# Kernel tuning notes

Measured on AMD Instinct MI355X. Metric: run time of the kernel, lower is better.

## Reference

```python
import jax, jax.numpy as jnp
import numpy as np

N, E, EP, D = 50000, 600000, 200000, 128
L = 3  # gnn layers


def _w(k, shape):
    # Kaiming-ish init: scale by 1/sqrt(fan_in)
    return jax.random.normal(k, shape, jnp.float32) / jnp.sqrt(jnp.float32(shape[-2]))


def setup_inputs() -> dict:
    key = jax.random.key(0)
    ks = jax.random.split(key, 20)
    x = jax.random.normal(ks[0], (N, D), jnp.float32)
    edge_attr = jax.random.normal(ks[1], (E, 1), jnp.float32)
    edge_index = jax.random.randint(ks[2], (2, E), 0, N, jnp.int64)
    predict_edge_index = jax.random.randint(ks[3], (2, EP), 0, N, jnp.int64)
    return {
        "x": x,
        "edge_attr": edge_attr,
        "edge_index": edge_index,
        "predict_edge_index": predict_edge_index,
        # SAGEConv params per layer: out = lin_l(mean_aggr) + lin_r(x); lin_r has no bias
        "Wl": _w(ks[4], (L, D, D)),
        "bl": jnp.zeros((L, D), jnp.float32),
        "Wr": _w(ks[5], (L, D, D)),
        # edge update MLPs: layer0 in=2D+1, layers 1..L-1 in=3D
        "euW0": _w(ks[6], (2 * D + 1, D)),
        "euB0": jnp.zeros((D,), jnp.float32),
        "euW": _w(ks[7], (L - 1, 3 * D, D)),
        "euB": jnp.zeros((L - 1, D), jnp.float32),
        # node post MLP
        "pW1": _w(ks[8], (D, D)), "pb1": jnp.zeros((D,), jnp.float32),
        "pW2": _w(ks[9], (D, D)), "pb2": jnp.zeros((D,), jnp.float32),
        # edge predict MLP (predict_mode=0: concat of two node embeddings)
        "qW1": _w(ks[10], (2 * D, D)), "qb1": jnp.zeros((D,), jnp.float32),
        "qW2": _w(ks[11], (D, 1)), "qb2": jnp.zeros((1,), jnp.float32),
    }


def reference(x, edge_attr, edge_index, predict_edge_index,
              Wl, bl, Wr, euW0, euB0, euW, euB,
              pW1, pb1, pW2, pb2, qW1, qb1, qW2, qb2):
    # dropout p=0.0 / eval mode -> identity
    src, dst = edge_index[0], edge_index[1]
    n = x.shape[0]
    deg = jax.ops.segment_sum(jnp.ones(src.shape, jnp.float32), dst, num_segments=n)
    deg = jnp.maximum(deg, 1.0)[:, None]
    for l in range(L):
        # SAGEConv: mean-aggregate source features at destinations
        aggr = jax.ops.segment_sum(x[src], dst, num_segments=n) / deg
        x = jax.nn.relu(aggr @ Wl[l] + bl[l] + x @ Wr[l])
        # edge update: gather endpoints, concat with edge_attr, Linear+ReLU (+outer relu no-op)
        cat = jnp.concatenate([x[src], x[dst], edge_attr], axis=-1)
        if l == 0:
            edge_attr = jax.nn.relu(cat @ euW0 + euB0)
        else:
            edge_attr = jax.nn.relu(cat @ euW[l - 1] + euB[l - 1])
    # node post MLP
    x = jax.nn.relu(x @ pW1 + pb1) @ pW2 + pb2
    # predict_mode=0: gather pair endpoints and score
    xi = x[predict_edge_index[0]]
    xj = x[predict_edge_index[1]]
    h = jnp.concatenate([xi, xj], axis=-1)
    y = jax.nn.relu(h @ qW1 + qb1) @ qW2 + qb2  # [EP, 1]
    return y
```

## Files before the change

kernel.cpp:

```cpp
#include <hip/hip_runtime.h>


typedef __attribute__((ext_vector_type(8))) short bf16x8;
typedef __attribute__((ext_vector_type(4))) float f32x4;

__device__ __forceinline__ unsigned short f2bf(float x) {
  unsigned u = __float_as_uint(x);
  u += 0x7fffu + ((u >> 16) & 1u);
  return (unsigned short)(u >> 16);
}
__device__ __forceinline__ float bf2f(unsigned short h) {
  return __uint_as_float(((unsigned)h) << 16);
}
__device__ __forceinline__ float lo16f(unsigned u) { return __uint_as_float(u << 16); }
__device__ __forceinline__ float hi16f(unsigned u) { return __uint_as_float(u & 0xffff0000u); }

__device__ __forceinline__ void gload_lds16(const void* g, void* l) {
  __builtin_amdgcn_global_load_lds(
      (const __attribute__((address_space(1))) unsigned int*)g,
      (__attribute__((address_space(3))) unsigned int*)l, 16, 0, 0);
}

__global__ void k_count(const int* __restrict__ dst, int* __restrict__ cnt, int E) {
  int i = blockIdx.x * blockDim.x + threadIdx.x;
  if (i < E) atomicAdd(&cnt[dst[i]], 1);
}

__global__ void k_scan1(const int* __restrict__ cnt, int* __restrict__ rs,
                        float* __restrict__ degf, int* __restrict__ bsum, int n) {
  __shared__ int wsum[16];
  __shared__ int wpre[16];
  const int tid = threadIdx.x;
  const int lane = tid & 63;
  const int wv = tid >> 6;
  int i = blockIdx.x * 1024 + tid;
  int v = (i < n) ? cnt[i] : 0;
  int s = v;
#pragma unroll
  for (int off = 1; off < 64; off <<= 1) {
    int t = __shfl_up(s, off);
    if (lane >= off) s += t;
  }
  if (lane == 63) wsum[wv] = s;
  __syncthreads();
  if (tid < 16) {
    int t = wsum[tid];
    int ss = t;
#pragma unroll
    for (int off = 1; off < 16; off <<= 1) {
      int u = __shfl_up(ss, off);
      if (tid >= off) ss += u;
    }
    wpre[tid] = ss - t;
  }
  __syncthreads();
  if (i < n) {
    rs[i] = s - v + wpre[wv];
    degf[i] = (float)(v > 0 ? v : 1);
  }
  if (tid == 1023) bsum[blockIdx.x] = wpre[15] + wsum[15];
}

__global__ void k_scan3(int* __restrict__ rs, const int* __restrict__ bsum,
                        int* __restrict__ cursor, int n, int nb) {
  __shared__ int boff_s[64];
  __shared__ int total_s;
  int tid = threadIdx.x;
  if (tid < 64) {
    int v = (tid < nb) ? bsum[tid] : 0;
    int s = v;
#pragma unroll
    for (int off = 1; off < 64; off <<= 1) {
      int t = __shfl_up(s, off);
      if (tid >= off) s += t;
    }
    boff_s[tid] = s - v;
    if (tid == 63) total_s = s;
  }
  __syncthreads();
  int i = blockIdx.x * blockDim.x + tid;
  if (i < n) {
    int r = rs[i] + boff_s[i >> 10];
    rs[i] = r;
    cursor[i] = r;
  }
  if (blockIdx.x == 0 && tid == 0) rs[n] = total_s;
}

__global__ void k_scatter(const int* __restrict__ src, const int* __restrict__ dst,
                          int* __restrict__ cursor, int* __restrict__ csr, int E) {
  int i = blockIdx.x * blockDim.x + threadIdx.x;
  if (i < E) {
    int p = atomicAdd(&cursor[dst[i]], 1);
    csr[p] = src[i];
  }
}

__global__ void k_split(const float* __restrict__ x, unsigned* __restrict__ X,
                        long n2) {
  long g = (long)blockIdx.x * blockDim.x + threadIdx.x;
  if (g >= n2) return;
  float2 v = ((const float2*)x)[g];
  unsigned short hx = f2bf(v.x), hy = f2bf(v.y);
  unsigned short lx = f2bf(v.x - bf2f(hx)), ly = f2bf(v.y - bf2f(hy));
  long row = g >> 6, p = g & 63;
  X[row * 128 + p] = (unsigned)hx | ((unsigned)hy << 16);
  X[row * 128 + 64 + p] = (unsigned)lx | ((unsigned)ly << 16);
}

__global__ void k_packAll(const float* __restrict__ Wl, const float* __restrict__ Wr,
                          const float* __restrict__ pW1, const float* __restrict__ pW2,
                          const float* __restrict__ qW1,
                          unsigned short* __restrict__ hi,
                          unsigned short* __restrict__ lo) {
  int gid = blockIdx.x * blockDim.x + threadIdx.x;
  if (gid >= 10 * 2048) return;
  int mat = gid >> 11;
  const float* Wm;
  if (mat < 3) Wm = Wl + (size_t)mat * 16384;
  else if (mat < 6) Wm = Wr + (size_t)(mat - 3) * 16384;
  else if (mat == 6) Wm = pW1;
  else if (mat == 7) Wm = pW2;
  else Wm = qW1 + (size_t)(mat - 8) * 16384;
  int lane = gid & 63;
  int f = (gid >> 6) & 31;
  int nt = f >> 2, ks = f & 3;
  int nn = nt * 16 + (lane & 15);
  int k0 = ks * 32 + 8 * (lane >> 4);
  size_t dst = (size_t)gid * 8;
#pragma unroll
  for (int r = 0; r < 8; ++r) {
    float w = Wm[(size_t)(k0 + r) * 128 + nn];
    unsigned short h = f2bf(w);
    hi[dst + r] = h;
    lo[dst + r] = f2bf(w - bf2f(h));
  }
}

__global__ void k_aggr(const unsigned short* __restrict__ X,
                       const int* __restrict__ csr, const int* __restrict__ rs,
                       const float* __restrict__ degf,
                       unsigned short* __restrict__ Bd, int n) {
  int gid = blockIdx.x * blockDim.x + threadIdx.x;
  int wid = gid >> 6, lane = gid & 63;
  if (wid >= n) return;
  int s = rs[wid], e = rs[wid + 1];
  const int h = lane >> 4;
  const int o16 = (lane & 15) * 8;
  float a0 = 0.f, a1 = 0.f, a2 = 0.f, a3 = 0.f;
  float a4 = 0.f, a5 = 0.f, a6 = 0.f, a7 = 0.f;
  int j = s;
  for (; j + 7 < e; j += 8) {
    int n0 = csr[j + h];
    int n1 = csr[j + 4 + h];
    uint4 v0 = *(const uint4*)(X + (size_t)n0 * 256 + o16);
    uint4 v1 = *(const uint4*)(X + (size_t)n1 * 256 + o16);
    a0 += lo16f(v0.x) + lo16f(v1.x);
    a1 += hi16f(v0.x) + hi16f(v1.x);
    a2 += lo16f(v0.y) + lo16f(v1.y);
    a3 += hi16f(v0.y) + hi16f(v1.y);
    a4 += lo16f(v0.z) + lo16f(v1.z);
    a5 += hi16f(v0.z) + hi16f(v1.z);
    a6 += lo16f(v0.w) + lo16f(v1.w);
    a7 += hi16f(v0.w) + hi16f(v1.w);
  }
  for (; j < e; j += 4) {
    int idx = j + h;
    bool ok = idx < e;
    int nn = ok ? csr[idx] : 0;
    uint4 v = *(const uint4*)(X + (size_t)nn * 256 + o16);
    float m = ok ? 1.f : 0.f;
    a0 += m * lo16f(v.x); a1 += m * hi16f(v.x);
    a2 += m * lo16f(v.y); a3 += m * hi16f(v.y);
    a4 += m * lo16f(v.z); a5 += m * hi16f(v.z);
    a6 += m * lo16f(v.w); a7 += m * hi16f(v.w);
  }
  a0 += __shfl_xor(a0, 16); a1 += __shfl_xor(a1, 16);
  a2 += __shfl_xor(a2, 16); a3 += __shfl_xor(a3, 16);
  a4 += __shfl_xor(a4, 16); a5 += __shfl_xor(a5, 16);
  a6 += __shfl_xor(a6, 16); a7 += __shfl_xor(a7, 16);
  a0 += __shfl_xor(a0, 32); a1 += __shfl_xor(a1, 32);
  a2 += __shfl_xor(a2, 32); a3 += __shfl_xor(a3, 32);
  a4 += __shfl_xor(a4, 32); a5 += __shfl_xor(a5, 32);
  a6 += __shfl_xor(a6, 32); a7 += __shfl_xor(a7, 32);
  if (lane < 16) {
    float inv = 1.0f / degf[wid];
    unsigned short h0 = f2bf(a0 * inv), h1 = f2bf(a1 * inv);
    unsigned short h2 = f2bf(a2 * inv), h3 = f2bf(a3 * inv);
    unsigned short h4 = f2bf(a4 * inv), h5 = f2bf(a5 * inv);
    unsigned short h6 = f2bf(a6 * inv), h7 = f2bf(a7 * inv);
    uint4 oh;
    oh.x = (unsigned)h0 | ((unsigned)h1 << 16);
    oh.y = (unsigned)h2 | ((unsigned)h3 << 16);
    oh.z = (unsigned)h4 | ((unsigned)h5 << 16);
    oh.w = (unsigned)h6 | ((unsigned)h7 << 16);
    *(uint4*)(Bd + (size_t)wid * 128 + o16) = oh;
  }
}

__device__ __forceinline__ void mm3term(f32x4 acc[8], const bf16x8 a_h[4],
                                        const bf16x8 a_l[4],
                                        const unsigned short* smh,
                                        const unsigned short* sml, int lane) {
#pragma unroll
  for (int ks = 0; ks < 4; ++ks)
#pragma unroll
    for (int nt = 0; nt < 8; ++nt) {
      const bf16x8 b_h = *(const bf16x8*)(smh + (nt * 4 + ks) * 512 + lane * 8);
      const bf16x8 b_l = *(const bf16x8*)(sml + (nt * 4 + ks) * 512 + lane * 8);
      acc[nt] = __builtin_amdgcn_mfma_f32_16x16x32_bf16(b_h, a_h[ks], acc[nt], 0, 0, 0);
      acc[nt] = __builtin_amdgcn_mfma_f32_16x16x32_bf16(b_h, a_l[ks], acc[nt], 0, 0, 0);
      acc[nt] = __builtin_amdgcn_mfma_f32_16x16x32_bf16(b_l, a_h[ks], acc[nt], 0, 0, 0);
    }
}

template <bool RELU>
__device__ __forceinline__ void t_store(const f32x4 acc[8], const float* bias,
                                        unsigned short* tw, int r16, int cq) {
#pragma unroll
  for (int nt = 0; nt < 8; ++nt) {
    int col = nt * 16 + cq;
    float4 bv = *(const float4*)(bias + col);
    float v0 = acc[nt][0] + bv.x, v1 = acc[nt][1] + bv.y;
    float v2 = acc[nt][2] + bv.z, v3 = acc[nt][3] + bv.w;
    if (RELU) {
      v0 = fmaxf(v0, 0.f); v1 = fmaxf(v1, 0.f);
      v2 = fmaxf(v2, 0.f); v3 = fmaxf(v3, 0.f);
    }
    unsigned short h0 = f2bf(v0), h1 = f2bf(v1), h2 = f2bf(v2), h3 = f2bf(v3);
    uint2 oh, ol;
    oh.x = (unsigned)h0 | ((unsigned)h1 << 16);
    oh.y = (unsigned)h2 | ((unsigned)h3 << 16);
    ol.x = (unsigned)f2bf(v0 - bf2f(h0)) | ((unsigned)f2bf(v1 - bf2f(h1)) << 16);
    ol.y = (unsigned)f2bf(v2 - bf2f(h2)) | ((unsigned)f2bf(v3 - bf2f(h3)) << 16);
    int idx = (r16 * 128 + col) ^ ((r16 & 7) << 3);
    *(uint2*)(tw + idx) = oh;
    *(uint2*)(tw + 2048 + idx) = ol;
  }
}

__device__ __forceinline__ void t_load(bf16x8 a_h[4], bf16x8 a_l[4],
                                       const unsigned short* tw, int r16, int kgrp) {
#pragma unroll
  for (int ks = 0; ks < 4; ++ks) {
    int idx = (r16 * 128 + ks * 32 + kgrp) ^ ((r16 & 7) << 3);
    a_h[ks] = *(const bf16x8*)(tw + idx);
    a_l[ks] = *(const bf16x8*)(tw + 2048 + idx);
  }
}

__global__ __launch_bounds__(512, 4) void k_gemm(
    const unsigned short* __restrict__ A0, const unsigned short* __restrict__ A1,
    const unsigned short* __restrict__ W0h, const unsigned short* __restrict__ W0l,
    const unsigned short* __restrict__ W1h, const unsigned short* __restrict__ W1l,
    const float* __restrict__ bias, unsigned short* __restrict__ O, int nrows) {
  __shared__ unsigned short smem[32768];
  unsigned short* smh = smem;
  unsigned short* sml = smem + 16384;

  const int tid = threadIdx.x;
  const int lane = tid & 63;
  const int wv = tid >> 6;
  const long row0 = ((long)blockIdx.x * 8 + wv) * 16;
  const bool active = row0 < nrows;
  const int kgrp = (lane >> 4) * 8;

  long r = row0 + (lane & 15);
  const long arow = (r < nrows) ? r : (long)(nrows - 1);

#pragma unroll
  for (int k = 0; k < 4; ++k) {
    int t = tid + k * 512;
    gload_lds16((const uint4*)W0h + t, (uint4*)smh + t);
    gload_lds16((const uint4*)W0l + t, (uint4*)sml + t);
  }

  bf16x8 a0h[4], a1h[4], a1l[4];
  if (active) {
#pragma unroll
    for (int ks = 0; ks < 4; ++ks) {
      a0h[ks] = *(const bf16x8*)(A0 + arow * 128 + ks * 32 + kgrp);
      a1h[ks] = *(const bf16x8*)(A1 + arow * 256 + ks * 32 + kgrp);
      a1l[ks] = *(const bf16x8*)(A1 + arow * 256 + 128 + ks * 32 + kgrp);
    }
  }

  f32x4 zero = {0.f, 0.f, 0.f, 0.f};
  f32x4 acc[8];
#pragma unroll
  for (int t = 0; t < 8; ++t) acc[t] = zero;

  __syncthreads();

  if (active) {
#pragma unroll
    for (int ks = 0; ks < 4; ++ks)
#pragma unroll
      for (int nt = 0; nt < 8; ++nt) {
        const bf16x8 b_h = *(const bf16x8*)(smh + (nt * 4 + ks) * 512 + lane * 8);
        const bf16x8 b_l = *(const bf16x8*)(sml + (nt * 4 + ks) * 512 + lane * 8);
        acc[nt] = __builtin_amdgcn_mfma_f32_16x16x32_bf16(b_h, a0h[ks], acc[nt], 0, 0, 0);
        acc[nt] = __builtin_amdgcn_mfma_f32_16x16x32_bf16(b_l, a0h[ks], acc[nt], 0, 0, 0);
      }
  }

  __syncthreads();
#pragma unroll
  for (int k = 0; k < 4; ++k) {
    int t = tid + k * 512;
    gload_lds16((const uint4*)W1h + t, (uint4*)smh + t);
    gload_lds16((const uint4*)W1l + t, (uint4*)sml + t);
  }
  __syncthreads();
  if (!active) return;

  mm3term(acc, a1h, a1l, smh, sml, lane);

  const int cq = (lane >> 4) * 4;
  const long row = row0 + (lane & 15);
  if (row >= nrows) return;
#pragma unroll
  for (int nt = 0; nt < 8; ++nt) {
    const int col = nt * 16 + cq;
    float4 bv = *(const float4*)(bias + col);
    float v0 = fmaxf(acc[nt][0] + bv.x, 0.f);
    float v1 = fmaxf(acc[nt][1] + bv.y, 0.f);
    float v2 = fmaxf(acc[nt][2] + bv.z, 0.f);
    float v3 = fmaxf(acc[nt][3] + bv.w, 0.f);
    unsigned short h0 = f2bf(v0), h1 = f2bf(v1), h2 = f2bf(v2), h3 = f2bf(v3);
    uint2 oh, ol;
    oh.x = (unsigned)h0 | ((unsigned)h1 << 16);
    oh.y = (unsigned)h2 | ((unsigned)h3 << 16);
    ol.x = (unsigned)f2bf(v0 - bf2f(h0)) | ((unsigned)f2bf(v1 - bf2f(h1)) << 16);
    ol.y = (unsigned)f2bf(v2 - bf2f(h2)) | ((unsigned)f2bf(v3 - bf2f(h3)) << 16);
    *(uint2*)(O + row * 256 + col) = oh;
    *(uint2*)(O + row * 256 + 128 + col) = ol;
  }
}

__global__ __launch_bounds__(512, 2) void k_post(
    const unsigned short* __restrict__ X,
    const unsigned short* __restrict__ W1h, const unsigned short* __restrict__ W1l,
    const unsigned short* __restrict__ W2h, const unsigned short* __restrict__ W2l,
    const unsigned short* __restrict__ W3h, const unsigned short* __restrict__ W3l,
    const unsigned short* __restrict__ W4h, const unsigned short* __restrict__ W4l,
    const float* __restrict__ b1, const float* __restrict__ b2,
    const float* __restrict__ b3, const float* __restrict__ b4,
    unsigned short* __restrict__ U, unsigned short* __restrict__ V, int nrows) {
  __shared__ unsigned short smem[32768];
  unsigned short* smh = smem;
  unsigned short* sml = smem + 16384;

  const int tid = threadIdx.x;
  const int lane = tid & 63;
  const int wv = tid >> 6;
  const long row0 = ((long)blockIdx.x * 8 + wv) * 16;
  const bool active = row0 < nrows;
  const int kgrp = (lane >> 4) * 8;
  const int r16 = lane & 15;
  const int cq = (lane >> 4) * 4;
  unsigned short* tw = smem + wv * 4096;

  long rr = row0 + r16;
  const long arow = (rr < nrows) ? rr : (long)(nrows - 1);
  const long row = row0 + r16;

#pragma unroll
  for (int k = 0; k < 4; ++k) {
    int t = tid + k * 512;
    gload_lds16((const uint4*)W1h + t, (uint4*)smh + t);
    gload_lds16((const uint4*)W1l + t, (uint4*)sml + t);
  }
  bf16x8 a_h[4], a_l[4];
  if (active) {
#pragma unroll
    for (int ks = 0; ks < 4; ++ks) {
      a_h[ks] = *(const bf16x8*)(X + arow * 256 + ks * 32 + kgrp);
      a_l[ks] = *(const bf16x8*)(X + arow * 256 + 128 + ks * 32 + kgrp);
    }
  }
  f32x4 zero = {0.f, 0.f, 0.f, 0.f};
  f32x4 acc[8];
#pragma unroll
  for (int t = 0; t < 8; ++t) acc[t] = zero;

  __syncthreads();
  if (active) mm3term(acc, a_h, a_l, smh, sml, lane);
  __syncthreads();

  if (active) {
    t_store<true>(acc, b1, tw, r16, cq);
    t_load(a_h, a_l, tw, r16, kgrp);
  }
  __syncthreads();

#pragma unroll
  for (int k = 0; k < 4; ++k) {
    int t = tid + k * 512;
    gload_lds16((const uint4*)W2h + t, (uint4*)smh + t);
    gload_lds16((const uint4*)W2l + t, (uint4*)sml + t);
  }
#pragma unroll
  for (int t = 0; t < 8; ++t) acc[t] = zero;
  __syncthreads();
  if (active) mm3term(acc, a_h, a_l, smh, sml, lane);
  __syncthreads();

  if (active) {
    t_store<false>(acc, b2, tw, r16, cq);
    t_load(a_h, a_l, tw, r16, kgrp);
  }
  __syncthreads();

#pragma unroll
  for (int k = 0; k < 4; ++k) {
    int t = tid + k * 512;
    gload_lds16((const uint4*)W3h + t, (uint4*)smh + t);
    gload_lds16((const uint4*)W3l + t, (uint4*)sml + t);
  }
#pragma unroll
  for (int t = 0; t < 8; ++t) acc[t] = zero;
  __syncthreads();
  if (active) mm3term(acc, a_h, a_l, smh, sml, lane);
  if (active && row < nrows) {
#pragma unroll
    for (int nt = 0; nt < 8; ++nt) {
      const int col = nt * 16 + cq;
      float4 bv = *(const float4*)(b3 + col);
      unsigned short h0 = f2bf(acc[nt][0] + bv.x), h1 = f2bf(acc[nt][1] + bv.y);
      unsigned short h2 = f2bf(acc[nt][2] + bv.z), h3 = f2bf(acc[nt][3] + bv.w);
      uint2 oh;
      oh.x = (unsigned)h0 | ((unsigned)h1 << 16);
      oh.y = (unsigned)h2 | ((unsigned)h3 << 16);
      *(uint2*)(U + row * 128 + col) = oh;
    }
  }
  __syncthreads();

#pragma unroll
  for (int k = 0; k < 4; ++k) {
    int t = tid + k * 512;
    gload_lds16((const uint4*)W4h + t, (uint4*)smh + t);
    gload_lds16((const uint4*)W4l + t, (uint4*)sml + t);
  }
#pragma unroll
  for (int t = 0; t < 8; ++t) acc[t] = zero;
  __syncthreads();
  if (!active || row >= nrows) return;
  mm3term(acc, a_h, a_l, smh, sml, lane);
#pragma unroll
  for (int nt = 0; nt < 8; ++nt) {
    const int col = nt * 16 + cq;
    float4 bv = *(const float4*)(b4 + col);
    unsigned short h0 = f2bf(acc[nt][0] + bv.x), h1 = f2bf(acc[nt][1] + bv.y);
    unsigned short h2 = f2bf(acc[nt][2] + bv.z), h3 = f2bf(acc[nt][3] + bv.w);
    uint2 oh;
    oh.x = (unsigned)h0 | ((unsigned)h1 << 16);
    oh.y = (unsigned)h2 | ((unsigned)h3 << 16);
    *(uint2*)(V + row * 128 + col) = oh;
  }
}

__global__ __launch_bounds__(256) void k_pair(
    const unsigned short* __restrict__ u, const unsigned short* __restrict__ v,
    const int* __restrict__ ps, const int* __restrict__ pd,
    const float* __restrict__ qW2, const float* __restrict__ qb2,
    float* __restrict__ out, int EP) {
  int gid = blockIdx.x * blockDim.x + threadIdx.x;
  long wid = gid >> 6;
  int lane = gid & 63;
  int sub = lane & 15, g = lane >> 4;
  long base = wid * 8;
  if (base >= EP) return;
  float4 q0 = *(const float4*)(qW2 + sub * 8);
  float4 q1 = *(const float4*)(qW2 + sub * 8 + 4);
  float qb = qb2[0];

  long p0 = base + g;
  long p1 = base + 4 + g;
  long c0 = (p0 < EP) ? p0 : (EP - 1);
  long c1 = (p1 < EP) ? p1 : (EP - 1);
  int i0 = ps[c0], j0 = pd[c0];
  int i1 = ps[c1], j1 = pd[c1];
  uint4 a0 = *(const uint4*)(u + (size_t)i0 * 128 + sub * 8);
  uint4 b0 = *(const uint4*)(v + (size_t)j0 * 128 + sub * 8);
  uint4 a1 = *(const uint4*)(u + (size_t)i1 * 128 + sub * 8);
  uint4 b1 = *(const uint4*)(v + (size_t)j1 * 128 + sub * 8);

  float s0, s1;
  {
    float t;
    t = fmaxf(lo16f(a0.x) + lo16f(b0.x), 0.f) * q0.x;
    t = fmaf(fmaxf(hi16f(a0.x) + hi16f(b0.x), 0.f), q0.y, t);
    t = fmaf(fmaxf(lo16f(a0.y) + lo16f(b0.y), 0.f), q0.z, t);
    t = fmaf(fmaxf(hi16f(a0.y) + hi16f(b0.y), 0.f), q0.w, t);
    t = fmaf(fmaxf(lo16f(a0.z) + lo16f(b0.z), 0.f), q1.x, t);
    t = fmaf(fmaxf(hi16f(a0.z) + hi16f(b0.z), 0.f), q1.y, t);
    t = fmaf(fmaxf(lo16f(a0.w) + lo16f(b0.w), 0.f), q1.z, t);
    t = fmaf(fmaxf(hi16f(a0.w) + hi16f(b0.w), 0.f), q1.w, t);
    s0 = t;
    t = fmaxf(lo16f(a1.x) + lo16f(b1.x), 0.f) * q0.x;
    t = fmaf(fmaxf(hi16f(a1.x) + hi16f(b1.x), 0.f), q0.y, t);
    t = fmaf(fmaxf(lo16f(a1.y) + lo16f(b1.y), 0.f), q0.z, t);
    t = fmaf(fmaxf(hi16f(a1.y) + hi16f(b1.y), 0.f), q0.w, t);
    t = fmaf(fmaxf(lo16f(a1.z) + lo16f(b1.z), 0.f), q1.x, t);
    t = fmaf(fmaxf(hi16f(a1.z) + hi16f(b1.z), 0.f), q1.y, t);
    t = fmaf(fmaxf(lo16f(a1.w) + lo16f(b1.w), 0.f), q1.z, t);
    t = fmaf(fmaxf(hi16f(a1.w) + hi16f(b1.w), 0.f), q1.w, t);
    s1 = t;
  }
#pragma unroll
  for (int m = 1; m < 16; m <<= 1) {
    s0 += __shfl_xor(s0, m);
    s1 += __shfl_xor(s1, m);
  }
  if (sub == 0) {
    if (p0 < EP) out[p0] = s0 + qb;
    if (p1 < EP) out[p1] = s1 + qb;
  }
}

extern "C" void kernel_launch(void* const* d_in, const int* in_sizes, int n_in,
                              void* d_out, int out_size, void* d_ws, size_t ws_size,
                              hipStream_t stream) {
  const float* x_in = (const float*)d_in[0];
  const int* ei = (const int*)d_in[2];
  const int* pe = (const int*)d_in[3];
  const float* Wl = (const float*)d_in[4];
  const float* bl = (const float*)d_in[5];
  const float* Wr = (const float*)d_in[6];
  const float* pW1 = (const float*)d_in[11];
  const float* pb1 = (const float*)d_in[12];
  const float* pW2 = (const float*)d_in[13];
  const float* pb2 = (const float*)d_in[14];
  const float* qW1 = (const float*)d_in[15];
  const float* qb1 = (const float*)d_in[16];
  const float* qW2 = (const float*)d_in[17];
  const float* qb2 = (const float*)d_in[18];

  const int N = in_sizes[0] / 128;
  const int E = in_sizes[2] / 2;
  const int EP = in_sizes[3] / 2;
  const int* e_src = ei;
  const int* e_dst = ei + E;
  const int* p_src = pe;
  const int* p_dst = pe + EP;

  char* ws = (char*)d_ws;
  size_t off = 0;
  auto alloc = [&](size_t bytes) {
    void* p = ws + off;
    off += (bytes + 511) & ~(size_t)511;
    return p;
  };
  unsigned short* X = (unsigned short*)alloc((size_t)N * 256 * 2);
  unsigned short* B = (unsigned short*)alloc((size_t)N * 256 * 2);
  int* deg_i = (int*)alloc((size_t)N * 4);
  int* rs = (int*)alloc((size_t)(N + 1) * 4);
  int* cursor = (int*)alloc((size_t)N * 4);
  float* degf = (float*)alloc((size_t)N * 4);
  int* csr = (int*)alloc((size_t)E * 4);
  int* bsum = (int*)alloc(64 * 4);
  unsigned short* Whi = (unsigned short*)alloc((size_t)10 * 16384 * 2);
  unsigned short* Wlo = (unsigned short*)alloc((size_t)10 * 16384 * 2);
  float* zerob = (float*)alloc(128 * 4);

  const size_t MS = 16384;
  const int nb = (N + 1023) / 1024;

  hipMemsetAsync(deg_i, 0, (size_t)N * 4, stream);
  hipMemsetAsync(zerob, 0, 128 * 4, stream);

  k_packAll<<<(10 * 2048 + 255) / 256, 256, 0, stream>>>(Wl, Wr, pW1, pW2, qW1,
                                                         Whi, Wlo);

  long n2 = (long)N * 64;
  k_split<<<(int)((n2 + 255) / 256), 256, 0, stream>>>(x_in, (unsigned*)X, n2);

  k_count<<<(E + 255) / 256, 256, 0, stream>>>(e_dst, deg_i, E);
  k_scan1<<<nb, 1024, 0, stream>>>(deg_i, rs, degf, bsum, N);
  k_scan3<<<(N + 255) / 256, 256, 0, stream>>>(rs, bsum, cursor, N, nb);
  k_scatter<<<(E + 255) / 256, 256, 0, stream>>>(e_src, e_dst, cursor, csr, E);

  const int gmm = (N + 127) / 128;
  const int agblocks = (N + 3) / 4;
  for (int l = 0; l < 3; ++l) {
    k_aggr<<<agblocks, 256, 0, stream>>>(X, csr, rs, degf, B, N);
    k_gemm<<<gmm, 512, 0, stream>>>(
        B, X, Whi + (size_t)l * MS, Wlo + (size_t)l * MS,
        Whi + (size_t)(3 + l) * MS, Wlo + (size_t)(3 + l) * MS,
        bl + (size_t)l * 128, X, N);
  }
  unsigned short* u = B;
  unsigned short* v = B + (size_t)N * 128;
  k_post<<<gmm, 512, 0, stream>>>(
      X, Whi + 6 * MS, Wlo + 6 * MS, Whi + 7 * MS, Wlo + 7 * MS,
      Whi + 8 * MS, Wlo + 8 * MS, Whi + 9 * MS, Wlo + 9 * MS,
      pb1, pb2, qb1, zerob, u, v, N);
  k_pair<<<(EP + 31) / 32, 256, 0, stream>>>(u, v, p_src, p_dst, qW2, qb2,
                                             (float*)d_out, EP);
}
```

Before: 287.9 us.

## Fuse mean aggregation into per-layer GEMM kernel with ping-pong buffers

Removes the separate aggregation kernel and has each GEMM thread gather and average its row's neighbor features directly in registers before the MFMA stage. Node features now ping-pong between two buffers, because the fused kernel reads neighbors while other blocks write outputs. This drops the intermediate aggregate buffer round-trip and one launch per layer. In exchange each lane walks a whole neighbor list serially with per-row load imbalance, and register pressure rises under the existing launch bounds.

```diff
diff --git a/kernel.cpp b/kernel.cpp
--- a/kernel.cpp
+++ b/kernel.cpp
@@ -137,67 +137,6 @@
   }
 }
 
-__global__ void k_aggr(const unsigned short* __restrict__ X,
-                       const int* __restrict__ csr, const int* __restrict__ rs,
-                       const float* __restrict__ degf,
-                       unsigned short* __restrict__ Bd, int n) {
-  int gid = blockIdx.x * blockDim.x + threadIdx.x;
-  int wid = gid >> 6, lane = gid & 63;
-  if (wid >= n) return;
-  int s = rs[wid], e = rs[wid + 1];
-  const int h = lane >> 4;
-  const int o16 = (lane & 15) * 8;
-  float a0 = 0.f, a1 = 0.f, a2 = 0.f, a3 = 0.f;
-  float a4 = 0.f, a5 = 0.f, a6 = 0.f, a7 = 0.f;
-  int j = s;
-  for (; j + 7 < e; j += 8) {
-    int n0 = csr[j + h];
-    int n1 = csr[j + 4 + h];
-    uint4 v0 = *(const uint4*)(X + (size_t)n0 * 256 + o16);
-    uint4 v1 = *(const uint4*)(X + (size_t)n1 * 256 + o16);
-    a0 += lo16f(v0.x) + lo16f(v1.x);
-    a1 += hi16f(v0.x) + hi16f(v1.x);
-    a2 += lo16f(v0.y) + lo16f(v1.y);
-    a3 += hi16f(v0.y) + hi16f(v1.y);
-    a4 += lo16f(v0.z) + lo16f(v1.z);
-    a5 += hi16f(v0.z) + hi16f(v1.z);
-    a6 += lo16f(v0.w) + lo16f(v1.w);
-    a7 += hi16f(v0.w) + hi16f(v1.w);
-  }
-  for (; j < e; j += 4) {
-    int idx = j + h;
-    bool ok = idx < e;
-    int nn = ok ? csr[idx] : 0;
-    uint4 v = *(const uint4*)(X + (size_t)nn * 256 + o16);
-    float m = ok ? 1.f : 0.f;
-    a0 += m * lo16f(v.x); a1 += m * hi16f(v.x);
-    a2 += m * lo16f(v.y); a3 += m * hi16f(v.y);
-    a4 += m * lo16f(v.z); a5 += m * hi16f(v.z);
-    a6 += m * lo16f(v.w); a7 += m * hi16f(v.w);
-  }
-  a0 += __shfl_xor(a0, 16); a1 += __shfl_xor(a1, 16);
-  a2 += __shfl_xor(a2, 16); a3 += __shfl_xor(a3, 16);
-  a4 += __shfl_xor(a4, 16); a5 += __shfl_xor(a5, 16);
-  a6 += __shfl_xor(a6, 16); a7 += __shfl_xor(a7, 16);
-  a0 += __shfl_xor(a0, 32); a1 += __shfl_xor(a1, 32);
-  a2 += __shfl_xor(a2, 32); a3 += __shfl_xor(a3, 32);
-  a4 += __shfl_xor(a4, 32); a5 += __shfl_xor(a5, 32);
-  a6 += __shfl_xor(a6, 32); a7 += __shfl_xor(a7, 32);
-  if (lane < 16) {
-    float inv = 1.0f / degf[wid];
-    unsigned short h0 = f2bf(a0 * inv), h1 = f2bf(a1 * inv);
-    unsigned short h2 = f2bf(a2 * inv), h3 = f2bf(a3 * inv);
-    unsigned short h4 = f2bf(a4 * inv), h5 = f2bf(a5 * inv);
-    unsigned short h6 = f2bf(a6 * inv), h7 = f2bf(a7 * inv);
-    uint4 oh;
-    oh.x = (unsigned)h0 | ((unsigned)h1 << 16);
-    oh.y = (unsigned)h2 | ((unsigned)h3 << 16);
-    oh.z = (unsigned)h4 | ((unsigned)h5 << 16);
-    oh.w = (unsigned)h6 | ((unsigned)h7 << 16);
-    *(uint4*)(Bd + (size_t)wid * 128 + o16) = oh;
-  }
-}
-
 __device__ __forceinline__ void mm3term(f32x4 acc[8], const bf16x8 a_h[4],
                                         const bf16x8 a_l[4],
                                         const unsigned short* smh,
@@ -249,11 +188,13 @@
   }
 }
 
-__global__ __launch_bounds__(512, 4) void k_gemm(
-    const unsigned short* __restrict__ A0, const unsigned short* __restrict__ A1,
+__global__ __launch_bounds__(512, 4) void k_layer(
+    const unsigned short* __restrict__ Xin,
+    const int* __restrict__ csr, const int* __restrict__ rs,
+    const float* __restrict__ degf,
     const unsigned short* __restrict__ W0h, const unsigned short* __restrict__ W0l,
     const unsigned short* __restrict__ W1h, const unsigned short* __restrict__ W1l,
-    const float* __restrict__ bias, unsigned short* __restrict__ O, int nrows) {
+    const float* __restrict__ bias, unsigned short* __restrict__ Xout, int nrows) {
   __shared__ unsigned short smem[32768];
   unsigned short* smh = smem;
   unsigned short* sml = smem + 16384;
@@ -263,10 +204,10 @@
   const int wv = tid >> 6;
   const long row0 = ((long)blockIdx.x * 8 + wv) * 16;
   const bool active = row0 < nrows;
+  const int r16 = lane & 15;
   const int kgrp = (lane >> 4) * 8;
-
-  long r = row0 + (lane & 15);
-  const long arow = (r < nrows) ? r : (long)(nrows - 1);
+  long rr = row0 + r16;
+  const long arow = (rr < nrows) ? rr : (long)(nrows - 1);
 
 #pragma unroll
   for (int k = 0; k < 4; ++k) {
@@ -275,13 +216,66 @@
     gload_lds16((const uint4*)W0l + t, (uint4*)sml + t);
   }
 
-  bf16x8 a0h[4], a1h[4], a1l[4];
+  float am[4][8];
+#pragma unroll
+  for (int ks = 0; ks < 4; ++ks)
+#pragma unroll
+    for (int d = 0; d < 8; ++d) am[ks][d] = 0.f;
+
+  bf16x8 a0h[4];
   if (active) {
+    int s = rs[arow], e = rs[arow + 1];
+    int j = s;
+    for (; j + 1 < e; j += 2) {
+      int n0 = csr[j], n1 = csr[j + 1];
+      const unsigned short* b0 = Xin + (size_t)n0 * 256 + kgrp;
+      const unsigned short* b1 = Xin + (size_t)n1 * 256 + kgrp;
+#pragma unroll
+      for (int ks = 0; ks < 4; ++ks) {
+        uint4 v0 = *(const uint4*)(b0 + ks * 32);
+        uint4 v1 = *(const uint4*)(b1 + ks * 32);
+        am[ks][0] += lo16f(v0.x) + lo16f(v1.x);
+        am[ks][1] += hi16f(v0.x) + hi16f(v1.x);
+        am[ks][2] += lo16f(v0.y) + lo16f(v1.y);
+        am[ks][3] += hi16f(v0.y) + hi16f(v1.y);
+        am[ks][4] += lo16f(v0.z) + lo16f(v1.z);
+        am[ks][5] += hi16f(v0.z) + hi16f(v1.z);
+        am[ks][6] += lo16f(v0.w) + lo16f(v1.w);
+        am[ks][7] += hi16f(v0.w) + hi16f(v1.w);
+      }
+    }
+    if (j < e) {
+      int n0 = csr[j];
+      const unsigned short* b0 = Xin + (size_t)n0 * 256 + kgrp;
+#pragma unroll
+      for (int ks = 0; ks < 4; ++ks) {
+        uint4 v0 = *(const uint4*)(b0 + ks * 32);
+        am[ks][0] += lo16f(v0.x); am[ks][1] += hi16f(v0.x);
+        am[ks][2] += lo16f(v0.y); am[ks][3] += hi16f(v0.y);
+        am[ks][4] += lo16f(v0.z); am[ks][5] += hi16f(v0.z);
+        am[ks][6] += lo16f(v0.w); am[ks][7] += hi16f(v0.w);
+      }
+    }
+    float inv = 1.0f / degf[arow];
 #pragma unroll
     for (int ks = 0; ks < 4; ++ks) {
-      a0h[ks] = *(const bf16x8*)(A0 + arow * 128 + ks * 32 + kgrp);
-      a1h[ks] = *(const bf16x8*)(A1 + arow * 256 + ks * 32 + kgrp);
-      a1l[ks] = *(const bf16x8*)(A1 + arow * 256 + 128 + ks * 32 + kgrp);
+      uint4 p;
+      p.x = (unsigned)f2bf(am[ks][0] * inv) | ((unsigned)f2bf(am[ks][1] * inv) << 16);
+      p.y = (unsigned)f2bf(am[ks][2] * inv) | ((unsigned)f2bf(am[ks][3] * inv) << 16);
+      p.z = (unsigned)f2bf(am[ks][4] * inv) | ((unsigned)f2bf(am[ks][5] * inv) << 16);
+      p.w = (unsigned)f2bf(am[ks][6] * inv) | ((unsigned)f2bf(am[ks][7] * inv) << 16);
+      union { uint4 u; bf16x8 b; } cvt;
+      cvt.u = p;
+      a0h[ks] = cvt.b;
+    }
+  }
+
+  bf16x8 a1h[4], a1l[4];
+  if (active) {
+#pragma unroll
+    for (int ks = 0; ks < 4; ++ks) {
+      a1h[ks] = *(const bf16x8*)(Xin + arow * 256 + ks * 32 + kgrp);
+      a1l[ks] = *(const bf16x8*)(Xin + arow * 256 + 128 + ks * 32 + kgrp);
     }
   }
 
@@ -317,7 +311,7 @@
   mm3term(acc, a1h, a1l, smh, sml, lane);
 
   const int cq = (lane >> 4) * 4;
-  const long row = row0 + (lane & 15);
+  const long row = row0 + r16;
   if (row >= nrows) return;
 #pragma unroll
   for (int nt = 0; nt < 8; ++nt) {
@@ -333,8 +327,8 @@
     oh.y = (unsigned)h2 | ((unsigned)h3 << 16);
     ol.x = (unsigned)f2bf(v0 - bf2f(h0)) | ((unsigned)f2bf(v1 - bf2f(h1)) << 16);
     ol.y = (unsigned)f2bf(v2 - bf2f(h2)) | ((unsigned)f2bf(v3 - bf2f(h3)) << 16);
-    *(uint2*)(O + row * 256 + col) = oh;
-    *(uint2*)(O + row * 256 + 128 + col) = ol;
+    *(uint2*)(Xout + row * 256 + col) = oh;
+    *(uint2*)(Xout + row * 256 + 128 + col) = ol;
   }
 }
 
@@ -553,8 +547,8 @@
     off += (bytes + 511) & ~(size_t)511;
     return p;
   };
-  unsigned short* X = (unsigned short*)alloc((size_t)N * 256 * 2);
-  unsigned short* B = (unsigned short*)alloc((size_t)N * 256 * 2);
+  unsigned short* X0 = (unsigned short*)alloc((size_t)N * 256 * 2);
+  unsigned short* X1 = (unsigned short*)alloc((size_t)N * 256 * 2);
   int* deg_i = (int*)alloc((size_t)N * 4);
   int* rs = (int*)alloc((size_t)(N + 1) * 4);
   int* cursor = (int*)alloc((size_t)N * 4);
@@ -575,7 +569,7 @@
                                                          Whi, Wlo);
 
   long n2 = (long)N * 64;
-  k_split<<<(int)((n2 + 255) / 256), 256, 0, stream>>>(x_in, (unsigned*)X, n2);
+  k_split<<<(int)((n2 + 255) / 256), 256, 0, stream>>>(x_in, (unsigned*)X0, n2);
 
   k_count<<<(E + 255) / 256, 256, 0, stream>>>(e_dst, deg_i, E);
   k_scan1<<<nb, 1024, 0, stream>>>(deg_i, rs, degf, bsum, N);
@@ -583,18 +577,20 @@
   k_scatter<<<(E + 255) / 256, 256, 0, stream>>>(e_src, e_dst, cursor, csr, E);
 
   const int gmm = (N + 127) / 128;
-  const int agblocks = (N + 3) / 4;
+
+  unsigned short* Xi = X0;
+  unsigned short* Xo = X1;
   for (int l = 0; l < 3; ++l) {
-    k_aggr<<<agblocks, 256, 0, stream>>>(X, csr, rs, degf, B, N);
-    k_gemm<<<gmm, 512, 0, stream>>>(
-        B, X, Whi + (size_t)l * MS, Wlo + (size_t)l * MS,
+    k_layer<<<gmm, 512, 0, stream>>>(
+        Xi, csr, rs, degf, Whi + (size_t)l * MS, Wlo + (size_t)l * MS,
         Whi + (size_t)(3 + l) * MS, Wlo + (size_t)(3 + l) * MS,
-        bl + (size_t)l * 128, X, N);
-  }
-  unsigned short* u = B;
-  unsigned short* v = B + (size_t)N * 128;
+        bl + (size_t)l * 128, Xo, N);
+    unsigned short* t = Xi; Xi = Xo; Xo = t;
+  }
+  unsigned short* u = Xo;
+  unsigned short* v = Xo + (size_t)N * 128;
   k_post<<<gmm, 512, 0, stream>>>(
-      X, Whi + 6 * MS, Wlo + 6 * MS, Whi + 7 * MS, Wlo + 7 * MS,
+      Xi, Whi + 6 * MS, Wlo + 6 * MS, Whi + 7 * MS, Wlo + 7 * MS,
       Whi + 8 * MS, Wlo + 8 * MS, Whi + 9 * MS, Wlo + 9 * MS,
       pb1, pb2, qb1, zerob, u, v, N);
   k_pair<<<(EP + 31) / 32, 256, 0, stream>>>(u, v, p_src, p_dst, qW2, qb2,
```

Result: no change. 282.6 us, median of 4 (-1.8%).
